# Kernel tuning notes

Measured on AMD Instinct MI355X. Metric: run time of the kernel, lower is better.

The kernel has to match this reference:

```python
import jax, jax.numpy as jnp
import numpy as np

N_HEADS = 8


def setup_inputs() -> dict:
    key = jax.random.key(0)
    ks = jax.random.split(key, 6)
    B, T, D = 8192, 64, 128
    s = 1.0 / np.sqrt(D)
    return {
        "center": jax.random.normal(ks[0], (B, D), dtype=jnp.float32),
        "neighbors": jax.random.normal(ks[1], (B, T, D), dtype=jnp.float32),
        "W_Q": jax.random.normal(ks[2], (D, D), dtype=jnp.float32) * s,
        "W_K": jax.random.normal(ks[3], (D, D), dtype=jnp.float32) * s,
        "W_V": jax.random.normal(ks[4], (D, D), dtype=jnp.float32) * s,
        "W_O": jax.random.normal(ks[5], (D, D), dtype=jnp.float32) * s,
    }


def reference(center, neighbors, W_Q, W_K, W_V, W_O):
    # center: [B, D], neighbors: [B, T, D]
    B, D = center.shape
    H = N_HEADS
    hd = D // H
    scale = hd ** -0.5
    # tokens = [center] ++ neighbors -> [B, 1+T, D]
    tokens = jnp.concatenate([center[:, None, :], neighbors], axis=1)
    # Only the center row of the attention output is used, so only the
    # center query is needed (math identical to the torch module's out[:, 0]).
    q = (center @ W_Q).reshape(B, H, hd)                 # [B, H, hd]
    K = (tokens @ W_K).reshape(B, -1, H, hd)             # [B, 1+T, H, hd]
    V = (tokens @ W_V).reshape(B, -1, H, hd)             # [B, 1+T, H, hd]
    scores = jnp.einsum('bhd,bthd->bht', q, K) * scale   # [B, H, 1+T]
    attn = jax.nn.softmax(scores, axis=-1)
    out = jnp.einsum('bht,bthd->bhd', attn, V).reshape(B, D)
    return out @ W_O
```

## Files before the change

kernel.cpp:

```cpp
#include <hip/hip_runtime.h>
#include <hip/hip_bf16.h>
#include <math.h>

namespace {

constexpr int D  = 128;
constexpr int TN = 64;
constexpr int NB = 8;

typedef _Float16 h2 __attribute__((ext_vector_type(2)));

__device__ __forceinline__ unsigned pack_h2(float a, float b) {
    h2 v; v.x = (_Float16)a; v.y = (_Float16)b;
    return __builtin_bit_cast(unsigned, v);
}
__device__ __forceinline__ float2 unp_h2(unsigned u) {
    h2 v = __builtin_bit_cast(h2, u);
    return make_float2((float)v.x, (float)v.y);
}
__device__ __forceinline__ float fdot2f(unsigned a, unsigned b, float c) {
#if __has_builtin(__builtin_amdgcn_fdot2)
    return __builtin_amdgcn_fdot2(__builtin_bit_cast(h2, a),
                                  __builtin_bit_cast(h2, b), c, false);
#else
    const float2 fa = unp_h2(a), fb = unp_h2(b);
    return fmaf(fa.x, fb.x, fmaf(fa.y, fb.y, c));
#endif
}


__global__ __launch_bounds__(256)
void k0_nm(const float* __restrict__ WQ, const float* __restrict__ WK,
           const float* __restrict__ WV, const float* __restrict__ WO,
           unsigned* __restrict__ N2, unsigned* __restrict__ M2)
{
    const int t = blockIdx.x * 256 + threadIdx.x;
    {
        const int kk = t >> 10, col = t & 1023;
        const int h = col >> 7, d = col & 127;
        const float* wq0 = WQ + (size_t)(2 * kk) * D + h * 16;
        const float* wq1 = wq0 + D;
        const float* wk  = WK + (size_t)d * D + h * 16;
        float a0 = 0.f, a1 = 0.f;
        #pragma unroll
        for (int j = 0; j < 16; ++j) {
            a0 = fmaf(wq0[j], wk[j], a0);
            a1 = fmaf(wq1[j], wk[j], a1);
        }
        N2[t] = pack_h2(0.25f * a0, 0.25f * a1);
    }
    {
        const int kk = t >> 7, e = t & 127;
        const int k0 = 2 * kk;
        const int h = k0 >> 7, d = k0 & 127;
        const float* wv0 = WV + (size_t)d * D + h * 16;
        const float* wv1 = wv0 + D;
        const float* wo  = WO + (size_t)(h * 16) * D + e;
        float b0 = 0.f, b1 = 0.f;
        #pragma unroll
        for (int j = 0; j < 16; ++j) {
            const float w_ = wo[(size_t)j * D];
            b0 = fmaf(wv0[j], w_, b0);
            b1 = fmaf(wv1[j], w_, b1);
        }
        M2[t] = pack_h2(b0, b1);
    }
}

__global__ __launch_bounds__(256, 2)
void k_fused(const float* __restrict__ center, const float* __restrict__ neighbors,
             const unsigned* __restrict__ N2, const unsigned* __restrict__ M2,
             float* __restrict__ out)
{
    __shared__ __align__(16) float nb_lds[TN * D / 2];
    __shared__ __align__(16) float qs8f[NB * 512];
    __shared__ __align__(16) unsigned c2u[NB * 64];
    __shared__ float P_lds[TN * 12];
    __shared__ float red_pc[8];

    const int tid = threadIdx.x;
    const int w   = tid >> 6;
    const int l   = tid & 63;
    const size_t rb = (size_t)blockIdx.x * NB;

    uint2* nbu  = (uint2*)nb_lds;
    uint2* qs8u = (uint2*)qs8f;

    {
        const int r = tid >> 5, f = tid & 31;
        const float4 g = ((const float4*)(center + (rb + r) * (size_t)D))[f];
        c2u[r * 64 + 2 * f]     = pack_h2(g.x, g.y);
        c2u[r * 64 + 2 * f + 1] = pack_h2(g.z, g.w);
    }
    __syncthreads();

    {
        const uint4* N2u4 = (const uint4*)N2;
        float4 acc[NB];
        #pragma unroll
        for (int r = 0; r < NB; ++r) acc[r] = make_float4(0.f, 0.f, 0.f, 0.f);

        #pragma unroll 4
        for (int kk = 0; kk < 64; ++kk) {
            const uint4 u = N2u4[(size_t)kk * 256 + tid];
            #pragma unroll
            for (int r = 0; r < NB; ++r) {
                const unsigned cp = c2u[r * 64 + kk];
                acc[r].x = fdot2f(cp, u.x, acc[r].x);
                acc[r].y = fdot2f(cp, u.y, acc[r].y);
                acc[r].z = fdot2f(cp, u.z, acc[r].z);
                acc[r].w = fdot2f(cp, u.w, acc[r].w);
            }
        }
        const int fc = tid & 31;
        const int qslot = (tid & ~31) | (((fc & 7) << 2) | (fc >> 3));
        #pragma unroll
        for (int r = 0; r < NB; ++r)
            qs8u[r * 256 + qslot] =
                make_uint2(pack_h2(acc[r].x, acc[r].y), pack_h2(acc[r].z, acc[r].w));
    }

    float4 st[8];
    {
        const float4* g0 = (const float4*)(neighbors + rb * TN * D);
        #pragma unroll
        for (int i = 0; i < 8; ++i) st[i] = g0[i * 256 + tid];
    }
    __syncthreads();

    #pragma unroll 1
    for (int bb = 0; bb < NB; ++bb) {
        #pragma unroll
        for (int i = 0; i < 8; ++i) {
            const int fi = i * 256 + tid;
            const int t  = fi >> 5;
            const int fc = fi & 31;
            nbu[(t << 5) | (fc ^ (t & 7))] =
                make_uint2(pack_h2(st[i].x, st[i].y), pack_h2(st[i].z, st[i].w));
        }
        __syncthreads();

        if (bb + 1 < NB) {
            const float4* gn = (const float4*)(neighbors + (rb + bb + 1) * TN * D);
            #pragma unroll
            for (int i = 0; i < 8; ++i) st[i] = gn[i * 256 + tid];
        }

        const uint2*    nb2 = (const uint2*)nb_lds;
        const uint2*    qku = qs8u + bb * 256;
        const unsigned* cb2 = c2u + bb * 64;

        const int tg = l & 15;
        const int q  = l >> 4;
        const int h0 = 2 * w;

        float sc0[4] = {0.f, 0.f, 0.f, 0.f};
        float sc1[4] = {0.f, 0.f, 0.f, 0.f};
        float s0a = 0.f, s0b = 0.f;
        #pragma unroll
        for (int jj = 0; jj < 8; ++jj) {
            const int rfc = (jj << 2) | q;
            const int fc  = (q << 3) | jj;
            const uint2 kv0p = qku[h0 * 32 + rfc];
            const uint2 kv1p = qku[(h0 + 1) * 32 + rfc];
            const unsigned cpa = cb2[2 * fc], cpb = cb2[2 * fc + 1];
            s0a = fdot2f(cpa, kv0p.x, fdot2f(cpb, kv0p.y, s0a));
            s0b = fdot2f(cpa, kv1p.x, fdot2f(cpb, kv1p.y, s0b));
            #pragma unroll
            for (int k = 0; k < 4; ++k) {
                const int t = tg + (k << 4);
                const uint2 u = nb2[(t << 5) | (fc ^ (t & 7))];
                sc0[k] = fdot2f(u.x, kv0p.x, fdot2f(u.y, kv0p.y, sc0[k]));
                sc1[k] = fdot2f(u.x, kv1p.x, fdot2f(u.y, kv1p.y, sc1[k]));
            }
        }
        #pragma unroll
        for (int k = 0; k < 4; ++k) {
            sc0[k] += __shfl_xor(sc0[k], 16);  sc0[k] += __shfl_xor(sc0[k], 32);
            sc1[k] += __shfl_xor(sc1[k], 16);  sc1[k] += __shfl_xor(sc1[k], 32);
        }
        s0a += __shfl_xor(s0a, 16);  s0a += __shfl_xor(s0a, 32);
        s0b += __shfl_xor(s0b, 16);  s0b += __shfl_xor(s0b, 32);

        float m0 = fmaxf(fmaxf(sc0[0], sc0[1]), fmaxf(sc0[2], sc0[3]));
        float m1 = fmaxf(fmaxf(sc1[0], sc1[1]), fmaxf(sc1[2], sc1[3]));
        #pragma unroll
        for (int off = 8; off >= 1; off >>= 1) {
            m0 = fmaxf(m0, __shfl_xor(m0, off));
            m1 = fmaxf(m1, __shfl_xor(m1, off));
        }
        m0 = fmaxf(m0, s0a);
        m1 = fmaxf(m1, s0b);
        float e0v[4], e1v[4];
        float sum0 = 0.f, sum1 = 0.f;
        #pragma unroll
        for (int k = 0; k < 4; ++k) {
            e0v[k] = __expf(sc0[k] - m0);  sum0 += e0v[k];
            e1v[k] = __expf(sc1[k] - m1);  sum1 += e1v[k];
        }
        #pragma unroll
        for (int off = 8; off >= 1; off >>= 1) {
            sum0 += __shfl_xor(sum0, off);
            sum1 += __shfl_xor(sum1, off);
        }
        const float ec0 = __expf(s0a - m0);
        const float ec1 = __expf(s0b - m1);
        const float inv0 = 1.0f / (sum0 + ec0);
        const float inv1 = 1.0f / (sum1 + ec1);
        if (q == 0) {
            #pragma unroll
            for (int k = 0; k < 4; ++k) {
                const int t = tg + (k << 4);
                *reinterpret_cast<float2*>(&P_lds[t * 12 + h0]) =
                    make_float2(e0v[k] * inv0, e1v[k] * inv1);
            }
            if (tg == 0) {
                red_pc[h0]     = ec0 * inv0;
                red_pc[h0 + 1] = ec1 * inv1;
            }
        }
        __syncthreads();

        const int hl  = l >> 5;
        const int fc2 = l & 31;
        float4 pacc[4];
        #pragma unroll
        for (int j = 0; j < 4; ++j) pacc[j] = make_float4(0.f, 0.f, 0.f, 0.f);
        #pragma unroll
        for (int tt = 0; tt < 16; ++tt) {
            const int t = w * 16 + tt;
            const uint2 u = nb2[(t << 5) | (fc2 ^ (t & 7))];
            const float2 ta = unp_h2(u.x), tb = unp_h2(u.y);
            const float t0 = ta.x, t1 = ta.y, t2 = tb.x, t3 = tb.y;
            const float4 pv = ((const float4*)P_lds)[t * 3 + hl];
            pacc[0].x = fmaf(pv.x, t0, pacc[0].x); pacc[0].y = fmaf(pv.x, t1, pacc[0].y);
            pacc[0].z = fmaf(pv.x, t2, pacc[0].z); pacc[0].w = fmaf(pv.x, t3, pacc[0].w);
            pacc[1].x = fmaf(pv.y, t0, pacc[1].x); pacc[1].y = fmaf(pv.y, t1, pacc[1].y);
            pacc[1].z = fmaf(pv.y, t2, pacc[1].z); pacc[1].w = fmaf(pv.y, t3, pacc[1].w);
            pacc[2].x = fmaf(pv.z, t0, pacc[2].x); pacc[2].y = fmaf(pv.z, t1, pacc[2].y);
            pacc[2].z = fmaf(pv.z, t2, pacc[2].z); pacc[2].w = fmaf(pv.z, t3, pacc[2].w);
            pacc[3].x = fmaf(pv.w, t0, pacc[3].x); pacc[3].y = fmaf(pv.w, t1, pacc[3].y);
            pacc[3].z = fmaf(pv.w, t2, pacc[3].z); pacc[3].w = fmaf(pv.w, t3, pacc[3].w);
        }
        #pragma unroll
        for (int j = 0; j < 4; ++j)
            ((float4*)nb_lds)[w * 256 + (hl * 4 + j) * 32 + fc2] = pacc[j];
        __syncthreads();

        {
            const int hE = tid >> 5;
            const int fE = tid & 31;
            float4 sum = make_float4(0.f, 0.f, 0.f, 0.f);
            #pragma unroll
            for (int ww = 0; ww < 4; ++ww) {
                const float4 p = ((const float4*)nb_lds)[ww * 256 + hE * 32 + fE];
                sum.x += p.x; sum.y += p.y; sum.z += p.z; sum.w += p.w;
            }
            const float pc = red_pc[hE];
            const float2 ca = unp_h2(cb2[2 * fE]), cb = unp_h2(cb2[2 * fE + 1]);
            sum.x = fmaf(pc, ca.x, sum.x);
            sum.y = fmaf(pc, ca.y, sum.y);
            sum.z = fmaf(pc, cb.x, sum.z);
            sum.w = fmaf(pc, cb.y, sum.w);
            qs8u[bb * 256 + tid] =
                make_uint2(pack_h2(sum.x, sum.y), pack_h2(sum.z, sum.w));
        }
        __syncthreads();
    }

    {
        const int cg = tid & 31;
        const int kg = tid >> 5;
        const int c4i = cg << 2;
        const int kb2 = kg << 6;

        float4 acc[NB];
        #pragma unroll
        for (int r = 0; r < NB; ++r) acc[r] = make_float4(0.f, 0.f, 0.f, 0.f);

        const uint4* M2u4 = (const uint4*)M2;
        const unsigned* sp2 = (const unsigned*)qs8f;

        #pragma unroll 4
        for (int k2 = 0; k2 < 64; ++k2) {
            const int kk = kb2 + k2;
            const uint4 u = M2u4[(size_t)kk * 32 + cg];
            #pragma unroll
            for (int r = 0; r < NB; ++r) {
                const unsigned sv = sp2[r * 512 + kk];
                acc[r].x = fdot2f(sv, u.x, acc[r].x);
                acc[r].y = fdot2f(sv, u.y, acc[r].y);
                acc[r].z = fdot2f(sv, u.z, acc[r].z);
                acc[r].w = fdot2f(sv, u.w, acc[r].w);
            }
        }
        __syncthreads();
        float* baseW = (kg < 4) ? nb_lds : qs8f;
        const int kgm = kg & 3;
        #pragma unroll
        for (int r = 0; r < NB; ++r)
            *reinterpret_cast<float4*>(&baseW[(kgm * 8 + r) * 128 + c4i]) = acc[r];
        __syncthreads();

        {
            const int r = tid >> 5;
            float4 sum = make_float4(0.f, 0.f, 0.f, 0.f);
            #pragma unroll
            for (int g = 0; g < 8; ++g) {
                const float* bg = (g < 4) ? nb_lds : qs8f;
                const float4 p = *reinterpret_cast<const float4*>(
                    &bg[((g & 3) * 8 + r) * 128 + c4i]);
                sum.x += p.x; sum.y += p.y; sum.z += p.z; sum.w += p.w;
            }
            *reinterpret_cast<float4*>(out + (rb + r) * D + c4i) = sum;
        }
    }
}

}

extern "C" void kernel_launch(void* const* d_in, const int* in_sizes, int n_in,
                              void* d_out, int out_size, void* d_ws, size_t ws_size,
                              hipStream_t stream) {
    const float* center    = (const float*)d_in[0];
    const float* neighbors = (const float*)d_in[1];
    const float* WQ        = (const float*)d_in[2];
    const float* WK        = (const float*)d_in[3];
    const float* WV        = (const float*)d_in[4];
    const float* WO        = (const float*)d_in[5];
    float* outp            = (float*)d_out;

    const int B = in_sizes[0] / D;

    unsigned* N2 = (unsigned*)d_ws;
    unsigned* M2 = N2 + 64 * 1024;

    hipLaunchKernelGGL(k0_nm,   dim3(256),    dim3(256), 0, stream, WQ, WK, WV, WO, N2, M2);
    hipLaunchKernelGGL(k_fused, dim3(B / NB), dim3(256), 0, stream, center, neighbors, N2, M2, outp);
}
```

Before: 110.5 us.

## Use MFMA for center-query projection and output projection with transposed weight layouts

Replaces the scalar fdot2 loops that compute the per-batch query projection (center times the folded WQ·WK matrix) and the final output projection (attention result times the folded WV·WO matrix) with 16x16x32 f16 MFMA instructions. The weight precompute kernel now writes transposed, 8-wide packed layouts to match the MFMA operand format, and runs with fewer blocks. Only 8 of the 16 MFMA batch columns hold real rows, so half of the matrix-core work is padding. The cross-warp LDS reduction and its extra barriers for the output stage are removed.

```diff
diff --git a/kernel.cpp b/kernel.cpp
--- a/kernel.cpp
+++ b/kernel.cpp
@@ -8,7 +8,10 @@
 constexpr int TN = 64;
 constexpr int NB = 8;
 
-typedef _Float16 h2 __attribute__((ext_vector_type(2)));
+typedef _Float16 h2  __attribute__((ext_vector_type(2)));
+typedef _Float16 v8h __attribute__((ext_vector_type(8)));
+typedef float    v4f __attribute__((ext_vector_type(4)));
+typedef unsigned uv4 __attribute__((ext_vector_type(4)));
 
 __device__ __forceinline__ unsigned pack_h2(float a, float b) {
     h2 v; v.x = (_Float16)a; v.y = (_Float16)b;
@@ -27,49 +30,58 @@
     return fmaf(fa.x, fb.x, fmaf(fa.y, fb.y, c));
 #endif
 }
+__device__ __forceinline__ int rot32(int fc) { return ((fc & 7) << 2) | (fc >> 3); }
+__device__ __forceinline__ v8h as_h8(uv4 u) { return __builtin_bit_cast(v8h, u); }
 
 
 __global__ __launch_bounds__(256)
 void k0_nm(const float* __restrict__ WQ, const float* __restrict__ WK,
            const float* __restrict__ WV, const float* __restrict__ WO,
-           unsigned* __restrict__ N2, unsigned* __restrict__ M2)
+           unsigned* __restrict__ NT, unsigned* __restrict__ MT)
 {
     const int t = blockIdx.x * 256 + threadIdx.x;
     {
-        const int kk = t >> 10, col = t & 1023;
+        const int col = t >> 4, k8 = t & 15;
         const int h = col >> 7, d = col & 127;
-        const float* wq0 = WQ + (size_t)(2 * kk) * D + h * 16;
-        const float* wq1 = wq0 + D;
-        const float* wk  = WK + (size_t)d * D + h * 16;
-        float a0 = 0.f, a1 = 0.f;
-        #pragma unroll
-        for (int j = 0; j < 16; ++j) {
-            a0 = fmaf(wq0[j], wk[j], a0);
-            a1 = fmaf(wq1[j], wk[j], a1);
-        }
-        N2[t] = pack_h2(0.25f * a0, 0.25f * a1);
-    }
-    {
-        const int kk = t >> 7, e = t & 127;
-        const int k0 = 2 * kk;
-        const int h = k0 >> 7, d = k0 & 127;
-        const float* wv0 = WV + (size_t)d * D + h * 16;
-        const float* wv1 = wv0 + D;
-        const float* wo  = WO + (size_t)(h * 16) * D + e;
-        float b0 = 0.f, b1 = 0.f;
-        #pragma unroll
-        for (int j = 0; j < 16; ++j) {
-            const float w_ = wo[(size_t)j * D];
-            b0 = fmaf(wv0[j], w_, b0);
-            b1 = fmaf(wv1[j], w_, b1);
-        }
-        M2[t] = pack_h2(b0, b1);
+        const float* wk = WK + (size_t)d * D + h * 16;
+        float a[8];
+        #pragma unroll
+        for (int jj = 0; jj < 8; ++jj) {
+            const int k = k8 * 8 + jj;
+            const float* wq = WQ + (size_t)k * D + h * 16;
+            float s = 0.f;
+            #pragma unroll
+            for (int j = 0; j < 16; ++j) s = fmaf(wq[j], wk[j], s);
+            a[jj] = 0.25f * s;
+        }
+        uv4 o;
+        o[0] = pack_h2(a[0], a[1]); o[1] = pack_h2(a[2], a[3]);
+        o[2] = pack_h2(a[4], a[5]); o[3] = pack_h2(a[6], a[7]);
+        ((uv4*)NT)[col * 16 + k8] = o;
+    }
+    {
+        const int e = t >> 7, k8 = t & 127;
+        const int h = k8 >> 4, d0 = (k8 * 8) & 127;
+        const float* wo = WO + (size_t)(h * 16) * D + e;
+        float b[8];
+        #pragma unroll
+        for (int jj = 0; jj < 8; ++jj) {
+            const float* wv = WV + (size_t)(d0 + jj) * D + h * 16;
+            float s = 0.f;
+            #pragma unroll
+            for (int j = 0; j < 16; ++j) s = fmaf(wv[j], wo[(size_t)j * D], s);
+            b[jj] = s;
+        }
+        uv4 o;
+        o[0] = pack_h2(b[0], b[1]); o[1] = pack_h2(b[2], b[3]);
+        o[2] = pack_h2(b[4], b[5]); o[3] = pack_h2(b[6], b[7]);
+        ((uv4*)MT)[e * 128 + k8] = o;
     }
 }
 
 __global__ __launch_bounds__(256, 2)
 void k_fused(const float* __restrict__ center, const float* __restrict__ neighbors,
-             const unsigned* __restrict__ N2, const unsigned* __restrict__ M2,
+             const unsigned* __restrict__ NT, const unsigned* __restrict__ MT,
              float* __restrict__ out)
 {
     __shared__ __align__(16) float nb_lds[TN * D / 2];
@@ -95,29 +107,30 @@
     __syncthreads();
 
     {
-        const uint4* N2u4 = (const uint4*)N2;
-        float4 acc[NB];
-        #pragma unroll
-        for (int r = 0; r < NB; ++r) acc[r] = make_float4(0.f, 0.f, 0.f, 0.f);
-
-        #pragma unroll 4
-        for (int kk = 0; kk < 64; ++kk) {
-            const uint4 u = N2u4[(size_t)kk * 256 + tid];
-            #pragma unroll
-            for (int r = 0; r < NB; ++r) {
-                const unsigned cp = c2u[r * 64 + kk];
-                acc[r].x = fdot2f(cp, u.x, acc[r].x);
-                acc[r].y = fdot2f(cp, u.y, acc[r].y);
-                acc[r].z = fdot2f(cp, u.z, acc[r].z);
-                acc[r].w = fdot2f(cp, u.w, acc[r].w);
-            }
-        }
-        const int fc = tid & 31;
-        const int qslot = (tid & ~31) | (((fc & 7) << 2) | (fc >> 3));
-        #pragma unroll
-        for (int r = 0; r < NB; ++r)
-            qs8u[r * 256 + qslot] =
-                make_uint2(pack_h2(acc[r].x, acc[r].y), pack_h2(acc[r].z, acc[r].w));
+        const uv4* NTv = (const uv4*)NT;
+        const uv4* cbv = (const uv4*)c2u;
+        uv4 bfr[4];
+        #pragma unroll
+        for (int kk = 0; kk < 4; ++kk)
+            bfr[kk] = cbv[(l & 7) * 16 + kk * 4 + (l >> 4)];
+
+        #pragma unroll 2
+        for (int t = 0; t < 16; ++t) {
+            const int col = (w * 16 + t) * 16 + (l & 15);
+            v4f acc = {0.f, 0.f, 0.f, 0.f};
+            #pragma unroll
+            for (int kk = 0; kk < 4; ++kk) {
+                const uv4 av = NTv[col * 16 + kk * 4 + (l >> 4)];
+                acc = __builtin_amdgcn_mfma_f32_16x16x32_f16(as_h8(av), as_h8(bfr[kk]), acc, 0, 0, 0);
+            }
+            const int batch = l & 15;
+            if (batch < NB) {
+                const int d0 = (w * 16 + t) * 16 + (l >> 4) * 4;
+                const int h = d0 >> 7, fc = (d0 & 127) >> 2;
+                qs8u[batch * 256 + h * 32 + rot32(fc)] =
+                    make_uint2(pack_h2(acc[0], acc[1]), pack_h2(acc[2], acc[3]));
+            }
+        }
     }
 
     float4 st[8];
@@ -269,50 +282,28 @@
     }
 
     {
-        const int cg = tid & 31;
-        const int kg = tid >> 5;
-        const int c4i = cg << 2;
-        const int kb2 = kg << 6;
-
-        float4 acc[NB];
-        #pragma unroll
-        for (int r = 0; r < NB; ++r) acc[r] = make_float4(0.f, 0.f, 0.f, 0.f);
-
-        const uint4* M2u4 = (const uint4*)M2;
-        const unsigned* sp2 = (const unsigned*)qs8f;
-
-        #pragma unroll 4
-        for (int k2 = 0; k2 < 64; ++k2) {
-            const int kk = kb2 + k2;
-            const uint4 u = M2u4[(size_t)kk * 32 + cg];
-            #pragma unroll
-            for (int r = 0; r < NB; ++r) {
-                const unsigned sv = sp2[r * 512 + kk];
-                acc[r].x = fdot2f(sv, u.x, acc[r].x);
-                acc[r].y = fdot2f(sv, u.y, acc[r].y);
-                acc[r].z = fdot2f(sv, u.z, acc[r].z);
-                acc[r].w = fdot2f(sv, u.w, acc[r].w);
-            }
-        }
-        __syncthreads();
-        float* baseW = (kg < 4) ? nb_lds : qs8f;
-        const int kgm = kg & 3;
-        #pragma unroll
-        for (int r = 0; r < NB; ++r)
-            *reinterpret_cast<float4*>(&baseW[(kgm * 8 + r) * 128 + c4i]) = acc[r];
-        __syncthreads();
-
-        {
-            const int r = tid >> 5;
-            float4 sum = make_float4(0.f, 0.f, 0.f, 0.f);
-            #pragma unroll
-            for (int g = 0; g < 8; ++g) {
-                const float* bg = (g < 4) ? nb_lds : qs8f;
-                const float4 p = *reinterpret_cast<const float4*>(
-                    &bg[((g & 3) * 8 + r) * 128 + c4i]);
-                sum.x += p.x; sum.y += p.y; sum.z += p.z; sum.w += p.w;
-            }
-            *reinterpret_cast<float4*>(out + (rb + r) * D + c4i) = sum;
+        const uv4* MTv = (const uv4*)MT;
+        const uv4* spv = (const uv4*)qs8f;
+        v4f acc0 = {0.f, 0.f, 0.f, 0.f};
+        v4f acc1 = {0.f, 0.f, 0.f, 0.f};
+        const int ec0 = (2 * w) * 16 + (l & 15);
+        const int ec1 = (2 * w + 1) * 16 + (l & 15);
+
+        #pragma unroll 2
+        for (int step = 0; step < 32; ++step) {
+            const uv4 bv = spv[(l & 7) * 128 + step * 4 + (l >> 4)];
+            const uv4 a0 = MTv[ec0 * 128 + step * 4 + (l >> 4)];
+            const uv4 a1 = MTv[ec1 * 128 + step * 4 + (l >> 4)];
+            acc0 = __builtin_amdgcn_mfma_f32_16x16x32_f16(as_h8(a0), as_h8(bv), acc0, 0, 0, 0);
+            acc1 = __builtin_amdgcn_mfma_f32_16x16x32_f16(as_h8(a1), as_h8(bv), acc1, 0, 0, 0);
+        }
+        const int batch = l & 15;
+        if (batch < NB) {
+            const int e0 = (2 * w) * 16 + (l >> 4) * 4;
+            const int e1 = (2 * w + 1) * 16 + (l >> 4) * 4;
+            float* orow = out + (rb + batch) * (size_t)D;
+            *reinterpret_cast<float4*>(orow + e0) = make_float4(acc0[0], acc0[1], acc0[2], acc0[3]);
+            *reinterpret_cast<float4*>(orow + e1) = make_float4(acc1[0], acc1[1], acc1[2], acc1[3]);
         }
     }
 }
@@ -332,9 +323,9 @@
 
     const int B = in_sizes[0] / D;
 
-    unsigned* N2 = (unsigned*)d_ws;
-    unsigned* M2 = N2 + 64 * 1024;
-
-    hipLaunchKernelGGL(k0_nm,   dim3(256),    dim3(256), 0, stream, WQ, WK, WV, WO, N2, M2);
-    hipLaunchKernelGGL(k_fused, dim3(B / NB), dim3(256), 0, stream, center, neighbors, N2, M2, outp);
-}
+    unsigned* NT = (unsigned*)d_ws;
+    unsigned* MT = NT + 1024 * 64;
+
+    hipLaunchKernelGGL(k0_nm,   dim3(64),     dim3(256), 0, stream, WQ, WK, WV, WO, NT, MT);
+    hipLaunchKernelGGL(k_fused, dim3(B / NB), dim3(256), 0, stream, center, neighbors, NT, MT, outp);
+}
```

Result: slower. 124.5 us (+12.6%).
